# Performance work log

Measured on AMD Instinct MI355X. Metric: run time of the kernel, lower is better.

## Reference

```python
import jax, jax.numpy as jnp
import numpy as np

B, P, ENC, EMB, DEC, ATT, V = 64, 196, 512, 512, 512, 512, 10000
CLS_E, NCLS = 512, 200
MAX_LEN = 52
MAX_T = MAX_LEN - 1  # decode steps = max(caption_lengths) - 1


def setup_inputs() -> dict:
    key = jax.random.key(0)
    ks = jax.random.split(key, 24)
    s = 0.02
    u = lambda k, shp: jax.random.uniform(k, shp, jnp.float32, -0.1, 0.1)
    n = lambda k, shp: jax.random.normal(k, shp, jnp.float32) * s
    cap_len = jax.random.randint(ks[2], (B, 1), 2, MAX_LEN + 1)
    cap_len = cap_len.at[0, 0].set(MAX_LEN)  # ensure max decode length is static MAX_T
    return {
        "encoder_out": jax.random.normal(ks[0], (B, P, ENC), jnp.float32),
        "encoded_captions": jax.random.randint(ks[1], (B, MAX_LEN), 0, V),
        "caption_lengths": cap_len,
        "class_k": jax.random.randint(ks[3], (B, 1), 0, NCLS),
        "emb_W": u(ks[4], (V, EMB)),
        "cls_emb_W": u(ks[5], (NCLS, CLS_E)),
        "enc_att_W": n(ks[6], (ENC, ATT)), "enc_att_b": jnp.zeros((ATT,), jnp.float32),
        "dec_att_W": n(ks[7], (DEC, ATT)), "dec_att_b": jnp.zeros((ATT,), jnp.float32),
        "full_att_w": n(ks[8], (ATT,)), "full_att_b": jnp.zeros((), jnp.float32),
        "init_h_W": n(ks[9], (ENC + CLS_E, DEC)), "init_h_b": jnp.zeros((DEC,), jnp.float32),
        "init_c_W": n(ks[10], (ENC + CLS_E, DEC)), "init_c_b": jnp.zeros((DEC,), jnp.float32),
        "f_beta_W": n(ks[11], (DEC, ENC)), "f_beta_b": jnp.zeros((ENC,), jnp.float32),
        "lstm_Wih": n(ks[12], (4 * DEC, EMB + ENC + CLS_E)),
        "lstm_Whh": n(ks[13], (4 * DEC, DEC)),
        "lstm_bih": jnp.zeros((4 * DEC,), jnp.float32),
        "lstm_bhh": jnp.zeros((4 * DEC,), jnp.float32),
        "fc_W": u(ks[14], (DEC, V)), "fc_b": jnp.zeros((V,), jnp.float32),
    }


def reference(encoder_out, encoded_captions, caption_lengths, class_k,
              emb_W, cls_emb_W, enc_att_W, enc_att_b, dec_att_W, dec_att_b,
              full_att_w, full_att_b, init_h_W, init_h_b, init_c_W, init_c_b,
              f_beta_W, f_beta_b, lstm_Wih, lstm_Whh, lstm_bih, lstm_bhh,
              fc_W, fc_b):
    # Sort by descending caption length (torch: caption_lengths.sort(descending=True))
    lens = caption_lengths[:, 0]
    sort_ind = jnp.argsort(-lens)
    lens_s = lens[sort_ind]
    enc = encoder_out[sort_ind]              # [B,P,ENC]
    caps = encoded_captions[sort_ind]        # [B,L]
    embs = emb_W[caps]                       # [B,L,EMB]
    # NOTE: original code does NOT sort class_k -- faithful to that.
    cls_emb = cls_emb_W[class_k[:, 0]]       # [B,CLS_E] (class_embedding[:,0,:])
    dec_len = lens_s - 1                     # decode_lengths

    init_in = jnp.concatenate([enc.mean(axis=1), cls_emb], axis=1)
    h = init_in @ init_h_W + init_h_b        # [B,DEC]
    c = init_in @ init_c_W + init_c_b
    att1 = enc @ enc_att_W + enc_att_b       # [B,P,ATT] (same every step in torch)

    def step(carry, xs):
        h, c = carry
        emb_t, t = xs                        # emb_t: [B,EMB]
        active = (t < dec_len)[:, None]      # ragged batch_size_t truncation as mask
        # attention
        att2 = h @ dec_att_W + dec_att_b
        e = jnp.einsum('bpa,a->bp', jax.nn.relu(att1 + att2[:, None, :]), full_att_w) + full_att_b
        alpha = jax.nn.softmax(e, axis=1)
        awe = jnp.einsum('bpe,bp->be', enc, alpha)
        gate = jax.nn.sigmoid(h @ f_beta_W + f_beta_b)
        awe = gate * awe
        # LSTMCell (torch gate order: i, f, g, o)
        x = jnp.concatenate([emb_t, awe, cls_emb], axis=1)
        gates = x @ lstm_Wih.T + lstm_bih + h @ lstm_Whh.T + lstm_bhh
        i_, f_, g_, o_ = jnp.split(gates, 4, axis=1)
        c_new = jax.nn.sigmoid(f_) * c + jax.nn.sigmoid(i_) * jnp.tanh(g_)
        h_new = jax.nn.sigmoid(o_) * jnp.tanh(c_new)
        # dropout is inference-mode identity
        pred = jnp.where(active, h_new @ fc_W + fc_b, 0.0)
        h = jnp.where(active, h_new, h)
        c = jnp.where(active, c_new, c)
        return (h, c), pred

    xs = (embs[:, :MAX_T].transpose(1, 0, 2), jnp.arange(MAX_T))
    _, preds = jax.lax.scan(step, (h, c), xs)
    predictions = preds.transpose(1, 0, 2)   # [B,MAX_T,V]
    return predictions, caps, dec_len, sort_ind
```

## Files before the change

kernel.cpp:

```cpp
#include <hip/hip_runtime.h>
#include <cstddef>
#include <cstdint>
#include <math.h>

#define BB 64
#define PP 196
#define ENCD 512
#define DECD 512
#define ATTD 512
#define VOC 10000
#define CLSE 512
#define MAXLEN 52
#define MAXT 51
#define G4 2048
#define XDIM 1536

#define OFF_PRED 0
#define OFF_CAPS (BB * MAXT * VOC)
#define OFF_DECLEN (OFF_CAPS + BB * MAXLEN)
#define OFF_SORT (OFF_DECLEN + BB)

static constexpr size_t W_SORT   = 0;
static constexpr size_t W_DECLEN = 64;
static constexpr size_t W_CAPS   = 128;
static constexpr size_t W_CLS    = 3584;
static constexpr size_t W_H      = W_CLS + BB * CLSE;
static constexpr size_t W_C      = W_H + BB * DECD;
static constexpr size_t W_ININ   = W_C + BB * DECD;
static constexpr size_t W_Z      = W_ININ + BB * 1024;
static constexpr size_t W_AWE    = W_Z + BB * 3072;
static constexpr size_t W_CLSPRE = W_AWE + BB * ENCD;
static constexpr size_t W_W1P    = W_CLSPRE + BB * G4;
static constexpr size_t W_W2P    = W_W1P + (size_t)256 * 12 * 512;
static constexpr size_t W_HALL   = W_W2P + (size_t)256 * 8 * 1024;
static constexpr size_t W_ATT1   = W_HALL + (size_t)BB * MAXT * DECD;
static constexpr size_t W_CNT    = W_ATT1 + (size_t)BB * PP * ATTD;
static constexpr size_t W_PAWE   = W_CNT + 3264;

__device__ __forceinline__ float sigm(float x) { return 1.f / (1.f + expf(-x)); }

__device__ __forceinline__ double cohLd(const double* p) {
    return __hip_atomic_load(p, __ATOMIC_RELAXED, __HIP_MEMORY_SCOPE_AGENT);
}
__device__ __forceinline__ float cohLdF(const float* p) {
    return __hip_atomic_load(p, __ATOMIC_RELAXED, __HIP_MEMORY_SCOPE_AGENT);
}
__device__ __forceinline__ void cohSt(double* p, double v) {
    __hip_atomic_store(p, v, __ATOMIC_RELAXED, __HIP_MEMORY_SCOPE_AGENT);
}
__device__ __forceinline__ void cohStF(float* p, float v) {
    __hip_atomic_store(p, v, __ATOMIC_RELAXED, __HIP_MEMORY_SCOPE_AGENT);
}

__global__ void setup_kernel(const int* __restrict__ cap_len, float* __restrict__ out,
                             int* __restrict__ sortind, int* __restrict__ declen,
                             int* __restrict__ cnt) {
    __shared__ int sl[BB];
    int i = threadIdx.x;
    for (int k = i; k < 3264; k += 64) cnt[k] = 0;
    sl[i] = cap_len[i];
    __syncthreads();
    int li = sl[i];
    int rank = 0;
    for (int j = 0; j < BB; j++) {
        int lj = sl[j];
        rank += (lj > li) || (lj == li && j < i);
    }
    sortind[rank] = i;
    declen[rank] = li - 1;
    out[OFF_SORT + rank] = (float)i;
    out[OFF_DECLEN + rank] = (float)(li - 1);
}

__global__ void gather_kernel(const int* __restrict__ ecaps, const int* __restrict__ classk,
                              const float* __restrict__ clsW, const int* __restrict__ sortind,
                              int* __restrict__ caps_i, float* __restrict__ cls,
                              float* __restrict__ out) {
    int idx = blockIdx.x * 256 + threadIdx.x;
    if (idx < BB * MAXLEN) {
        int b = idx / MAXLEN, t2 = idx - b * MAXLEN;
        int sb = sortind[b];
        int v = ecaps[sb * MAXLEN + t2];
        caps_i[idx] = v;
        out[OFF_CAPS + idx] = (float)v;
    }
    int j = idx - BB * MAXLEN;
    if (j >= 0 && j < BB * CLSE) {
        int row = j >> 9, k = j & 511;
        int ck = classk[row];
        cls[j] = clsW[ck * CLSE + k];
    }
}

__global__ void mean_cls_kernel(const float* __restrict__ enc, const float* __restrict__ cls,
                                const int* __restrict__ sortind, float* __restrict__ initin) {
    int b = blockIdx.x;
    int sb = sortind[b];
    for (int k = threadIdx.x; k < ENCD; k += 256) {
        const float* ep = enc + (size_t)sb * PP * ENCD + k;
        float s = 0.f;
        for (int p = 0; p < PP; p++) s += ep[(size_t)p * ENCD];
        initin[b * 1024 + k] = s * (1.f / 196.f);
        initin[b * 1024 + 512 + k] = cls[b * CLSE + k];
    }
}

__global__ void init_hc_kernel(const float* __restrict__ initin,
                               const float* __restrict__ hW, const float* __restrict__ hb,
                               const float* __restrict__ cW, const float* __restrict__ cb,
                               float* __restrict__ h, float* __restrict__ c) {
    int gid = blockIdx.x * 256 + threadIdx.x;
    int j = gid & 511, b = (gid >> 9) & 63, which = gid >> 15;
    const float* W = which ? cW : hW;
    const float* bias = which ? cb : hb;
    const float* x = initin + b * 1024;
    float acc = bias[j];
    for (int k = 0; k < 1024; k++) acc += x[k] * W[(size_t)k * 512 + j];
    (which ? c : h)[b * 512 + j] = acc;
}

__global__ void pack_w1p_kernel(const float* __restrict__ dA, const float* __restrict__ fB,
                                const float* __restrict__ whh, float* __restrict__ W1p) {
    int gid = blockIdx.x * 256 + threadIdx.x;
    int k = gid & 511, cc = (gid >> 9) % 12, jb = gid / (512 * 12);
    int q = jb * 12 + cc;
    float v;
    if (q < 512) v = dA[k * 512 + q];
    else if (q < 1024) v = fB[k * 512 + (q - 512)];
    else v = whh[(size_t)(q - 1024) * 512 + k];
    W1p[gid] = v;
}

__global__ void pack_w2p_kernel(const float* __restrict__ wih, float* __restrict__ W2p) {
    int gid = blockIdx.x * 256 + threadIdx.x;
    int k = gid & 1023, cc = (gid >> 10) & 7, jb = gid >> 13;
    int gcol = 512 * (cc >> 1) + 2 * jb + (cc & 1);
    W2p[gid] = wih[(size_t)gcol * XDIM + k];
}

__global__ __launch_bounds__(256)
void att1_kernel(const float* __restrict__ enc, const float* __restrict__ Wa,
                 const float* __restrict__ ba, const int* __restrict__ sortind,
                 float* __restrict__ att1) {
    __shared__ float As[16][66];
    __shared__ float Bs[16][64];
    int tid = threadIdx.x;
    int n0 = blockIdx.x * 64, m0 = blockIdx.y * 64;
    int tx = tid & 15, ty = tid >> 4;
    int lm = tid >> 2, lk4 = (tid & 3) * 4;
    int bkk = tid >> 4, bnn4 = (tid & 15) * 4;
    int gm = m0 + lm;
    int b = gm / PP, p = gm - b * PP;
    int sb = sortind[b];
    const float* arow = enc + ((size_t)sb * PP + p) * ENCD;
    float acc[4][4] = {};
    for (int k0 = 0; k0 < ENCD; k0 += 16) {
        float4 av = *(const float4*)(arow + k0 + lk4);
        float4 bv = *(const float4*)(Wa + (size_t)(k0 + bkk) * 512 + n0 + bnn4);
        __syncthreads();
        As[lk4 + 0][lm] = av.x; As[lk4 + 1][lm] = av.y;
        As[lk4 + 2][lm] = av.z; As[lk4 + 3][lm] = av.w;
        *(float4*)&Bs[bkk][bnn4] = bv;
        __syncthreads();
#pragma unroll
        for (int kk = 0; kk < 16; kk++) {
            float a[4], bq[4];
#pragma unroll
            for (int i = 0; i < 4; i++) a[i] = As[kk][ty * 4 + i];
#pragma unroll
            for (int jj = 0; jj < 4; jj++) bq[jj] = Bs[kk][tx * 4 + jj];
#pragma unroll
            for (int i = 0; i < 4; i++)
#pragma unroll
                for (int jj = 0; jj < 4; jj++) acc[i][jj] += a[i] * bq[jj];
        }
    }
#pragma unroll
    for (int i = 0; i < 4; i++) {
        int m = m0 + ty * 4 + i;
        int n = n0 + tx * 4;
        float4 o;
        o.x = acc[i][0] + ba[n + 0];
        o.y = acc[i][1] + ba[n + 1];
        o.z = acc[i][2] + ba[n + 2];
        o.w = acc[i][3] + ba[n + 3];
        *(float4*)(att1 + (size_t)m * ATTD + n) = o;
    }
}

__global__ __launch_bounds__(256)
void clspre_kernel(const float* __restrict__ cls, const float* __restrict__ wih,
                   const float* __restrict__ bih, const float* __restrict__ bhh,
                   float* __restrict__ clspre) {
    __shared__ float As[16][66];
    __shared__ float Bs[16][68];
    int tid = threadIdx.x;
    int n0 = blockIdx.x * 64;
    int tx = tid & 15, ty = tid >> 4;
    int lm = tid >> 2, lk4 = (tid & 3) * 4;
    int bnn = tid & 63, bkk4 = (tid >> 6) * 4;
    float acc[4][4] = {};
    for (int k0 = 0; k0 < 512; k0 += 16) {
        float4 av = *(const float4*)(cls + lm * CLSE + k0 + lk4);
        float4 bv = *(const float4*)(wih + (size_t)(n0 + bnn) * XDIM + 1024 + k0 + bkk4);
        __syncthreads();
        As[lk4 + 0][lm] = av.x; As[lk4 + 1][lm] = av.y;
        As[lk4 + 2][lm] = av.z; As[lk4 + 3][lm] = av.w;
        Bs[bkk4 + 0][bnn] = bv.x; Bs[bkk4 + 1][bnn] = bv.y;
        Bs[bkk4 + 2][bnn] = bv.z; Bs[bkk4 + 3][bnn] = bv.w;
        __syncthreads();
#pragma unroll
        for (int kk = 0; kk < 16; kk++) {
            float a[4], bq[4];
#pragma unroll
            for (int i = 0; i < 4; i++) a[i] = As[kk][ty * 4 + i];
#pragma unroll
            for (int jj = 0; jj < 4; jj++) bq[jj] = Bs[kk][tx * 4 + jj];
#pragma unroll
            for (int i = 0; i < 4; i++)
#pragma unroll
                for (int jj = 0; jj < 4; jj++) acc[i][jj] += a[i] * bq[jj];
        }
    }
#pragma unroll
    for (int i = 0; i < 4; i++) {
        int m = ty * 4 + i;
#pragma unroll
        for (int jj = 0; jj < 4; jj++) {
            int n = n0 + tx * 4 + jj;
            clspre[m * G4 + n] = acc[i][jj] + bih[n] + bhh[n];
        }
    }
}

__global__ __launch_bounds__(256)
void zstep_kernel(const float* __restrict__ hG, const float* __restrict__ W1p,
                  const float* __restrict__ dab, const float* __restrict__ fbb,
                  float* __restrict__ Zg) {
    const int j = blockIdx.x, tid = threadIdx.x;
    const int lane = tid & 63, wvid = tid >> 6;
    __shared__ float stage[64 * 132];
    __shared__ float W1res[12 * 516];

    for (int idx = tid; idx < 1536; idx += 256) {
        int cc = idx >> 7, pos = (idx & 127) << 2;
        *(float4*)&W1res[cc * 516 + pos] = *(const float4*)&W1p[(size_t)j * 6144 + cc * 512 + pos];
    }
    const int gc0 = j * 12 + wvid, gc1 = gc0 + 4, gc2 = gc0 + 8;
    const float bias0 = (gc0 < 512) ? dab[gc0] : ((gc0 < 1024) ? fbb[gc0 - 512] : 0.f);
    const float bias1 = (gc1 < 512) ? dab[gc1] : ((gc1 < 1024) ? fbb[gc1 - 512] : 0.f);
    const float bias2 = (gc2 < 512) ? dab[gc2] : ((gc2 < 1024) ? fbb[gc2 - 512] : 0.f);

    float a0 = 0.f, a1 = 0.f, a2 = 0.f;
    for (int ch = 0; ch < 4; ch++) {
        __syncthreads();
        {
            const float4* hp = (const float4*)(hG + ((size_t)lane << 9) + (ch << 7) + (wvid << 5));
            float4 tmp[8];
#pragma unroll
            for (int i = 0; i < 8; i++) tmp[i] = hp[i];
#pragma unroll
            for (int i = 0; i < 8; i++)
                *(float4*)&stage[lane * 132 + (wvid << 5) + (i << 2)] = tmp[i];
        }
        __syncthreads();
        const float* sp  = &stage[lane * 132];
        const float* w0p = &W1res[wvid * 516 + (ch << 7)];
        const float* w1p = &W1res[(wvid + 4) * 516 + (ch << 7)];
        const float* w2p = &W1res[(wvid + 8) * 516 + (ch << 7)];
#pragma unroll 8
        for (int kk = 0; kk < 128; kk += 4) {
            float4 av = *(const float4*)(sp + kk);
            float4 u0 = *(const float4*)(w0p + kk);
            float4 u1 = *(const float4*)(w1p + kk);
            float4 u2 = *(const float4*)(w2p + kk);
            a0 = fmaf(av.x, u0.x, fmaf(av.y, u0.y, fmaf(av.z, u0.z, fmaf(av.w, u0.w, a0))));
            a1 = fmaf(av.x, u1.x, fmaf(av.y, u1.y, fmaf(av.z, u1.z, fmaf(av.w, u1.w, a1))));
            a2 = fmaf(av.x, u2.x, fmaf(av.y, u2.y, fmaf(av.z, u2.z, fmaf(av.w, u2.w, a2))));
        }
    }
    Zg[lane * 3072 + gc0] = a0 + bias0;
    Zg[lane * 3072 + gc1] = a1 + bias1;
    Zg[lane * 3072 + gc2] = a2 + bias2;
}

__global__ __launch_bounds__(256)
void attq_kernel(const float* __restrict__ att1g, const float* __restrict__ encg,
                 const float* __restrict__ Zg, const float* __restrict__ fullw,
                 const float* __restrict__ fullb, const int* __restrict__ sortind,
                 const int* __restrict__ declen, float* __restrict__ paweG,
                 int* __restrict__ cntG, float* __restrict__ aweG, int t) {
    const int blk = blockIdx.x;
    const int b = blk >> 2, q = blk & 3;
    if (t >= declen[b]) return;
    const int tid = threadIdx.x;
    const int lane = tid & 63, wvid = tid >> 6;

    __shared__ float att2s[512];
    __shared__ float esS[52];
    __shared__ float redA[1], redB[1];
    __shared__ float pawe[4 * 520];
    __shared__ int finS;

    {
        float2 v = *(const float2*)&Zg[b * 3072 + 2 * tid];
        *(float2*)&att2s[2 * tid] = v;
    }
    __syncthreads();

    const float fbv = fullb[0];
    {
        float4 t0 = *(const float4*)&att2s[lane * 8];
        float4 t1 = *(const float4*)&att2s[lane * 8 + 4];
        float4 w0 = *(const float4*)&fullw[lane * 8];
        float4 w1 = *(const float4*)&fullw[lane * 8 + 4];
        const float* a1b = att1g + (size_t)b * PP * 512;
        for (int lp = wvid; lp < 49; lp += 4) {
            int p = 49 * q + lp;
            const float4* ar = (const float4*)(a1b + (size_t)p * 512) + lane * 2;
            float4 u0 = ar[0], u1 = ar[1];
            float s = fmaxf(u0.x + t0.x, 0.f) * w0.x + fmaxf(u0.y + t0.y, 0.f) * w0.y
                    + fmaxf(u0.z + t0.z, 0.f) * w0.z + fmaxf(u0.w + t0.w, 0.f) * w0.w
                    + fmaxf(u1.x + t1.x, 0.f) * w1.x + fmaxf(u1.y + t1.y, 0.f) * w1.y
                    + fmaxf(u1.z + t1.z, 0.f) * w1.z + fmaxf(u1.w + t1.w, 0.f) * w1.w;
#pragma unroll
            for (int off = 32; off; off >>= 1) s += __shfl_down(s, off, 64);
            if (lane == 0) esS[lp] = s + fbv;
        }
    }
    __syncthreads();
    if (tid < 64) {
        float v = (tid < 49) ? esS[tid] : -1e30f;
#pragma unroll
        for (int off = 32; off; off >>= 1) v = fmaxf(v, __shfl_down(v, off, 64));
        if (tid == 0) redA[0] = v;
    }
    __syncthreads();
    const float mq = redA[0];
    if (tid < 64) {
        float ev = (tid < 49) ? expf(esS[tid] - mq) : 0.f;
        float sv = ev;
#pragma unroll
        for (int off = 32; off; off >>= 1) sv += __shfl_down(sv, off, 64);
        if (tid == 0) redB[0] = sv;
        if (tid < 49) esS[tid] = ev;
    }
    __syncthreads();
    const float Sq = redB[0];

    const int sb = sortind[b];
    {
        float aw[8] = {};
        const float* encb = encg + (size_t)sb * PP * 512 + lane;
        for (int lp = wvid; lp < 49; lp += 4) {
            int p = 49 * q + lp;
            float al = esS[lp];
            const float* ep = encb + (size_t)p * 512;
#pragma unroll
            for (int i = 0; i < 8; i++) aw[i] = fmaf(al, ep[i << 6], aw[i]);
        }
#pragma unroll
        for (int i = 0; i < 8; i++) pawe[wvid * 520 + (i << 6) + lane] = aw[i];
    }
    __syncthreads();
    {
        const int k2 = 2 * tid;
        const int base = ((b << 2) + q) * 520;
        float s0 = pawe[k2] + pawe[520 + k2] + pawe[2 * 520 + k2] + pawe[3 * 520 + k2];
        float s1 = pawe[k2 + 1] + pawe[520 + k2 + 1] + pawe[2 * 520 + k2 + 1] + pawe[3 * 520 + k2 + 1];
        double d;
        *(float2*)&d = make_float2(s0, s1);
        cohSt((double*)&paweG[base + k2], d);
        if (tid == 0) {
            cohStF(&paweG[base + 512], Sq);
            cohStF(&paweG[base + 513], mq);
        }
    }
    __syncthreads();

    if (tid == 0) {
        int prev = __hip_atomic_fetch_add(&cntG[t * 64 + b], 1,
                                          __ATOMIC_RELAXED, __HIP_MEMORY_SCOPE_AGENT);
        finS = (prev == 3);
    }
    __syncthreads();
    if (finS) {
        float mv[4], sv[4];
#pragma unroll
        for (int qq = 0; qq < 4; qq++) {
            mv[qq] = cohLdF(&paweG[((b << 2) + qq) * 520 + 513]);
            sv[qq] = cohLdF(&paweG[((b << 2) + qq) * 520 + 512]);
        }
        float M = fmaxf(fmaxf(mv[0], mv[1]), fmaxf(mv[2], mv[3]));
        float f0 = expf(mv[0] - M), f1 = expf(mv[1] - M);
        float f2 = expf(mv[2] - M), f3 = expf(mv[3] - M);
        float inv = 1.f / (sv[0] * f0 + sv[1] * f1 + sv[2] * f2 + sv[3] * f3);
        const int k2 = 2 * tid;
        const double* pd = (const double*)paweG;
        float a0 = 0.f, a1 = 0.f;
        {
            double d0 = cohLd(pd + ((b << 2) + 0) * 260 + tid);
            double d1 = cohLd(pd + ((b << 2) + 1) * 260 + tid);
            double d2 = cohLd(pd + ((b << 2) + 2) * 260 + tid);
            double d3 = cohLd(pd + ((b << 2) + 3) * 260 + tid);
            float2 g0 = *(float2*)&d0, g1 = *(float2*)&d1;
            float2 g2 = *(float2*)&d2, g3 = *(float2*)&d3;
            a0 = g0.x * f0 + g1.x * f1 + g2.x * f2 + g3.x * f3;
            a1 = g0.y * f0 + g1.y * f1 + g2.y * f2 + g3.y * f3;
        }
        float2 gv = *(const float2*)&Zg[b * 3072 + 512 + k2];
        float2 o = make_float2(a0 * inv * sigm(gv.x), a1 * inv * sigm(gv.y));
        *(float2*)&aweG[b * 512 + k2] = o;
    }
}

__global__ __launch_bounds__(256)
void gatestep_kernel(const float* __restrict__ embW, const float* __restrict__ W2p,
                     const float* __restrict__ clspreg, const float* __restrict__ Zg,
                     const float* __restrict__ aweG, const int* __restrict__ caps_i,
                     const int* __restrict__ declen, float* __restrict__ hG,
                     float* __restrict__ cG, float* __restrict__ hall, int t) {
    const int j = blockIdx.x, tid = threadIdx.x;
    const int lane = tid & 63, wvid = tid >> 6;
    const int d0 = j * 2;
    __shared__ float stage[64 * 132];
    __shared__ float W2res[8 * 1028];
    __shared__ float Gs[8 * 66];
    __shared__ float hhS[64 * 8];
    __shared__ float CsS[64 * 8];
    __shared__ int capS[64];
    __shared__ int declen_s[64];

    for (int idx = tid; idx < 2048; idx += 256) {
        int cc = idx >> 8, pos = (idx & 255) << 2;
        *(float4*)&W2res[cc * 1028 + pos] = *(const float4*)&W2p[(size_t)j * 8192 + cc * 1024 + pos];
    }
    for (int idx = tid; idx < 512; idx += 256) {
        int r = idx >> 3, cc = idx & 7;
        CsS[idx] = clspreg[(r << 11) + ((cc >> 1) << 9) + d0 + (cc & 1)];
    }
    if (tid < 64) { capS[tid] = caps_i[tid * MAXLEN + t]; declen_s[tid] = declen[tid]; }
    {
        int r = tid >> 2, g = tid & 3;
        float2 v = *(const float2*)&Zg[r * 3072 + 1024 + (g << 9) + d0];
        hhS[(r << 3) + (g << 1)] = v.x;
        hhS[(r << 3) + (g << 1) + 1] = v.y;
    }

    float ac0 = 0.f, ac1 = 0.f;
    for (int ch = 0; ch < 8; ch++) {
        __syncthreads();
        {
            const float4* src = (ch < 4)
                ? (const float4*)(embW + ((size_t)capS[lane] << 9) + (ch << 7) + (wvid << 5))
                : (const float4*)(aweG + ((size_t)lane << 9) + ((ch - 4) << 7) + (wvid << 5));
            float4 tmp[8];
#pragma unroll
            for (int i = 0; i < 8; i++) tmp[i] = src[i];
#pragma unroll
            for (int i = 0; i < 8; i++)
                *(float4*)&stage[lane * 132 + (wvid << 5) + (i << 2)] = tmp[i];
        }
        __syncthreads();
        const float* sp  = &stage[lane * 132];
        const float* v0p = &W2res[wvid * 1028 + (ch << 7)];
        const float* v1p = &W2res[(wvid + 4) * 1028 + (ch << 7)];
#pragma unroll 8
        for (int kk = 0; kk < 128; kk += 4) {
            float4 av = *(const float4*)(sp + kk);
            float4 u0 = *(const float4*)(v0p + kk);
            float4 u1 = *(const float4*)(v1p + kk);
            ac0 = fmaf(av.x, u0.x, fmaf(av.y, u0.y, fmaf(av.z, u0.z, fmaf(av.w, u0.w, ac0))));
            ac1 = fmaf(av.x, u1.x, fmaf(av.y, u1.y, fmaf(av.z, u1.z, fmaf(av.w, u1.w, ac1))));
        }
    }
    Gs[wvid * 66 + lane]       = ac0 + CsS[(lane << 3) + wvid]     + hhS[(lane << 3) + wvid];
    Gs[(wvid + 4) * 66 + lane] = ac1 + CsS[(lane << 3) + wvid + 4] + hhS[(lane << 3) + wvid + 4];
    __syncthreads();
    if (tid < 128) {
        int r2 = tid & 63, dd = tid >> 6;
        if (t < declen_s[r2]) {
            float iv = Gs[(0 + dd) * 66 + r2];
            float fv = Gs[(2 + dd) * 66 + r2];
            float gv = Gs[(4 + dd) * 66 + r2];
            float ov = Gs[(6 + dd) * 66 + r2];
            float cold = cG[r2 * 512 + d0 + dd];
            float cn = sigm(fv) * cold + sigm(iv) * tanhf(gv);
            float hn = sigm(ov) * tanhf(cn);
            cG[r2 * 512 + d0 + dd] = cn;
            hG[r2 * 512 + d0 + dd] = hn;
            hall[((size_t)r2 * MAXT + t) * 512 + d0 + dd] = hn;
        }
    }
}

__global__ __launch_bounds__(256)
void fc_kernel(const float* __restrict__ hall, const float* __restrict__ fcW,
               const float* __restrict__ fcb, const int* __restrict__ declen,
               float* __restrict__ out) {
    __shared__ float As[16][66];
    __shared__ float Bs[16][68];
    int tid = threadIdx.x;
    int n0 = blockIdx.x * 64, m0 = blockIdx.y * 64;
    int tx = tid & 15, ty = tid >> 4;
    int lm = tid >> 2, lk4 = (tid & 3) * 4;
    int bkk = tid >> 4, bnn4 = (tid & 15) * 4;
    const float* arow = hall + (size_t)(m0 + lm) * DECD;
    bool nfull = (n0 + 64 <= VOC);
    float acc[4][4] = {};
    for (int k0 = 0; k0 < 512; k0 += 16) {
        float4 av = *(const float4*)(arow + k0 + lk4);
        float4 bv;
        if (nfull) {
            bv = *(const float4*)(fcW + (size_t)(k0 + bkk) * VOC + n0 + bnn4);
        } else {
            const float* bp = fcW + (size_t)(k0 + bkk) * VOC;
            int nb = n0 + bnn4;
            bv.x = (nb + 0 < VOC) ? bp[nb + 0] : 0.f;
            bv.y = (nb + 1 < VOC) ? bp[nb + 1] : 0.f;
            bv.z = (nb + 2 < VOC) ? bp[nb + 2] : 0.f;
            bv.w = (nb + 3 < VOC) ? bp[nb + 3] : 0.f;
        }
        __syncthreads();
        As[lk4 + 0][lm] = av.x; As[lk4 + 1][lm] = av.y;
        As[lk4 + 2][lm] = av.z; As[lk4 + 3][lm] = av.w;
        *(float4*)&Bs[bkk][bnn4] = bv;
        __syncthreads();
#pragma unroll
        for (int kk = 0; kk < 16; kk++) {
            float a[4], bq[4];
#pragma unroll
            for (int i = 0; i < 4; i++) a[i] = As[kk][ty * 4 + i];
#pragma unroll
            for (int jj = 0; jj < 4; jj++) bq[jj] = Bs[kk][tx * 4 + jj];
#pragma unroll
            for (int i = 0; i < 4; i++)
#pragma unroll
                for (int jj = 0; jj < 4; jj++) acc[i][jj] += a[i] * bq[jj];
        }
    }
#pragma unroll
    for (int i = 0; i < 4; i++) {
        int m = m0 + ty * 4 + i;
        int b = m / MAXT, t = m - b * MAXT;
        bool act = t < declen[b];
        int n = n0 + tx * 4;
        if (nfull) {
            float4 o;
            o.x = act ? acc[i][0] + fcb[n + 0] : 0.f;
            o.y = act ? acc[i][1] + fcb[n + 1] : 0.f;
            o.z = act ? acc[i][2] + fcb[n + 2] : 0.f;
            o.w = act ? acc[i][3] + fcb[n + 3] : 0.f;
            *(float4*)(out + (size_t)m * VOC + n) = o;
        } else {
#pragma unroll
            for (int jj = 0; jj < 4; jj++) {
                int nn = n + jj;
                if (nn < VOC) out[(size_t)m * VOC + nn] = act ? acc[i][jj] + fcb[nn] : 0.f;
            }
        }
    }
}

extern "C" void kernel_launch(void* const* d_in, const int* in_sizes, int n_in,
                              void* d_out, int out_size, void* d_ws, size_t ws_size,
                              hipStream_t stream) {
    const float* enc     = (const float*)d_in[0];
    const int*   ecaps   = (const int*)d_in[1];
    const int*   lens    = (const int*)d_in[2];
    const int*   classk  = (const int*)d_in[3];
    const float* embW    = (const float*)d_in[4];
    const float* clsW    = (const float*)d_in[5];
    const float* encattW = (const float*)d_in[6];
    const float* encattb = (const float*)d_in[7];
    const float* decattW = (const float*)d_in[8];
    const float* decattb = (const float*)d_in[9];
    const float* fullw   = (const float*)d_in[10];
    const float* fullb   = (const float*)d_in[11];
    const float* ihW     = (const float*)d_in[12];
    const float* ihb     = (const float*)d_in[13];
    const float* icW     = (const float*)d_in[14];
    const float* icb     = (const float*)d_in[15];
    const float* fbW     = (const float*)d_in[16];
    const float* fbb     = (const float*)d_in[17];
    const float* Wih     = (const float*)d_in[18];
    const float* Whh     = (const float*)d_in[19];
    const float* bih     = (const float*)d_in[20];
    const float* bhh     = (const float*)d_in[21];
    const float* fcW     = (const float*)d_in[22];
    const float* fcb     = (const float*)d_in[23];

    float* out = (float*)d_out;
    float* ws  = (float*)d_ws;
    int*   wsi = (int*)d_ws;

    int*   sortind = wsi + W_SORT;
    int*   declen  = wsi + W_DECLEN;
    int*   caps_i  = wsi + W_CAPS;
    float* cls     = ws + W_CLS;
    float* h       = ws + W_H;
    float* c       = ws + W_C;
    float* initin  = ws + W_ININ;
    float* Z       = ws + W_Z;
    float* awe     = ws + W_AWE;
    float* clspre  = ws + W_CLSPRE;
    float* W1p     = ws + W_W1P;
    float* W2p     = ws + W_W2P;
    float* hall    = ws + W_HALL;
    float* att1    = ws + W_ATT1;
    int*   cnt     = wsi + W_CNT;
    float* pawe    = ws + W_PAWE;

    setup_kernel<<<1, 64, 0, stream>>>(lens, out, sortind, declen, cnt);
    gather_kernel<<<141, 256, 0, stream>>>(ecaps, classk, clsW, sortind, caps_i, cls, out);
    mean_cls_kernel<<<BB, 256, 0, stream>>>(enc, cls, sortind, initin);
    init_hc_kernel<<<256, 256, 0, stream>>>(initin, ihW, ihb, icW, icb, h, c);
    pack_w1p_kernel<<<6144, 256, 0, stream>>>(decattW, fbW, Whh, W1p);
    pack_w2p_kernel<<<8192, 256, 0, stream>>>(Wih, W2p);
    att1_kernel<<<dim3(8, 196), 256, 0, stream>>>(enc, encattW, encattb, sortind, att1);
    clspre_kernel<<<32, 256, 0, stream>>>(cls, Wih, bih, bhh, clspre);

    for (int t = 0; t < MAXT; t++) {
        zstep_kernel<<<256, 256, 0, stream>>>(h, W1p, decattb, fbb, Z);
        attq_kernel<<<256, 256, 0, stream>>>(att1, enc, Z, fullw, fullb,
                                             sortind, declen, pawe, cnt, awe, t);
        gatestep_kernel<<<256, 256, 0, stream>>>(embW, W2p, clspre, Z, awe,
                                                 caps_i, declen, h, c, hall, t);
    }

    fc_kernel<<<dim3(157, 51), 256, 0, stream>>>(hall, fcW, fcb, declen, out);
}
```

Before: 3.914 ms.

## Precompute embedding gate contributions for all steps; prefetch staged chunks in step kernels

Adds an embpre kernel that computes the embedding part of the LSTM input projection for all decode steps up front as one batched GEMM, folding in the class and bias term. The per-step gate kernel then only handles the attention-weighted-encoding half, halving its weight staging and chunk loop. It also prefetches the next global chunk into registers while the current chunk is staged in zstep and gatestep, and switches the small GEMM kernels to float4 LDS reads with padded rows. The new path depends on the workspace being large enough, about 26 MB extra, and falls back to the old path otherwise.

```diff
diff --git a/kernel.cpp b/kernel.cpp
--- a/kernel.cpp
+++ b/kernel.cpp
@@ -36,6 +36,8 @@
 static constexpr size_t W_ATT1   = W_HALL + (size_t)BB * MAXT * DECD;
 static constexpr size_t W_CNT    = W_ATT1 + (size_t)BB * PP * ATTD;
 static constexpr size_t W_PAWE   = W_CNT + 3264;
+static constexpr size_t W_CPRE2  = W_PAWE + (size_t)BB * 4 * 520;
+static constexpr size_t W_END    = W_CPRE2 + (size_t)MAXT * BB * G4;
 
 __device__ __forceinline__ float sigm(float x) { return 1.f / (1.f + expf(-x)); }
 
@@ -142,7 +144,7 @@
 void att1_kernel(const float* __restrict__ enc, const float* __restrict__ Wa,
                  const float* __restrict__ ba, const int* __restrict__ sortind,
                  float* __restrict__ att1) {
-    __shared__ float As[16][66];
+    __shared__ float As[16][68];
     __shared__ float Bs[16][64];
     int tid = threadIdx.x;
     int n0 = blockIdx.x * 64, m0 = blockIdx.y * 64;
@@ -164,15 +166,16 @@
         __syncthreads();
 #pragma unroll
         for (int kk = 0; kk < 16; kk++) {
-            float a[4], bq[4];
-#pragma unroll
-            for (int i = 0; i < 4; i++) a[i] = As[kk][ty * 4 + i];
-#pragma unroll
-            for (int jj = 0; jj < 4; jj++) bq[jj] = Bs[kk][tx * 4 + jj];
-#pragma unroll
-            for (int i = 0; i < 4; i++)
-#pragma unroll
-                for (int jj = 0; jj < 4; jj++) acc[i][jj] += a[i] * bq[jj];
+            float4 a4 = *(const float4*)&As[kk][ty * 4];
+            float4 b4 = *(const float4*)&Bs[kk][tx * 4];
+            acc[0][0] = fmaf(a4.x, b4.x, acc[0][0]); acc[0][1] = fmaf(a4.x, b4.y, acc[0][1]);
+            acc[0][2] = fmaf(a4.x, b4.z, acc[0][2]); acc[0][3] = fmaf(a4.x, b4.w, acc[0][3]);
+            acc[1][0] = fmaf(a4.y, b4.x, acc[1][0]); acc[1][1] = fmaf(a4.y, b4.y, acc[1][1]);
+            acc[1][2] = fmaf(a4.y, b4.z, acc[1][2]); acc[1][3] = fmaf(a4.y, b4.w, acc[1][3]);
+            acc[2][0] = fmaf(a4.z, b4.x, acc[2][0]); acc[2][1] = fmaf(a4.z, b4.y, acc[2][1]);
+            acc[2][2] = fmaf(a4.z, b4.z, acc[2][2]); acc[2][3] = fmaf(a4.z, b4.w, acc[2][3]);
+            acc[3][0] = fmaf(a4.w, b4.x, acc[3][0]); acc[3][1] = fmaf(a4.w, b4.y, acc[3][1]);
+            acc[3][2] = fmaf(a4.w, b4.z, acc[3][2]); acc[3][3] = fmaf(a4.w, b4.w, acc[3][3]);
         }
     }
 #pragma unroll
@@ -192,7 +195,7 @@
 void clspre_kernel(const float* __restrict__ cls, const float* __restrict__ wih,
                    const float* __restrict__ bih, const float* __restrict__ bhh,
                    float* __restrict__ clspre) {
-    __shared__ float As[16][66];
+    __shared__ float As[16][68];
     __shared__ float Bs[16][68];
     int tid = threadIdx.x;
     int n0 = blockIdx.x * 64;
@@ -211,15 +214,16 @@
         __syncthreads();
 #pragma unroll
         for (int kk = 0; kk < 16; kk++) {
-            float a[4], bq[4];
-#pragma unroll
-            for (int i = 0; i < 4; i++) a[i] = As[kk][ty * 4 + i];
-#pragma unroll
-            for (int jj = 0; jj < 4; jj++) bq[jj] = Bs[kk][tx * 4 + jj];
-#pragma unroll
-            for (int i = 0; i < 4; i++)
-#pragma unroll
-                for (int jj = 0; jj < 4; jj++) acc[i][jj] += a[i] * bq[jj];
+            float4 a4 = *(const float4*)&As[kk][ty * 4];
+            float4 b4 = *(const float4*)&Bs[kk][tx * 4];
+            acc[0][0] = fmaf(a4.x, b4.x, acc[0][0]); acc[0][1] = fmaf(a4.x, b4.y, acc[0][1]);
+            acc[0][2] = fmaf(a4.x, b4.z, acc[0][2]); acc[0][3] = fmaf(a4.x, b4.w, acc[0][3]);
+            acc[1][0] = fmaf(a4.y, b4.x, acc[1][0]); acc[1][1] = fmaf(a4.y, b4.y, acc[1][1]);
+            acc[1][2] = fmaf(a4.y, b4.z, acc[1][2]); acc[1][3] = fmaf(a4.y, b4.w, acc[1][3]);
+            acc[2][0] = fmaf(a4.z, b4.x, acc[2][0]); acc[2][1] = fmaf(a4.z, b4.y, acc[2][1]);
+            acc[2][2] = fmaf(a4.z, b4.z, acc[2][2]); acc[2][3] = fmaf(a4.z, b4.w, acc[2][3]);
+            acc[3][0] = fmaf(a4.w, b4.x, acc[3][0]); acc[3][1] = fmaf(a4.w, b4.y, acc[3][1]);
+            acc[3][2] = fmaf(a4.w, b4.z, acc[3][2]); acc[3][3] = fmaf(a4.w, b4.w, acc[3][3]);
         }
     }
 #pragma unroll
@@ -230,6 +234,55 @@
             int n = n0 + tx * 4 + jj;
             clspre[m * G4 + n] = acc[i][jj] + bih[n] + bhh[n];
         }
+    }
+}
+
+__global__ __launch_bounds__(256)
+void embpre_kernel(const float* __restrict__ embW, const float* __restrict__ wih,
+                   const float* __restrict__ clspreg, const int* __restrict__ caps_i,
+                   float* __restrict__ cpre2) {
+    __shared__ float As[16][68];
+    __shared__ float Bs[16][68];
+    int tid = threadIdx.x;
+    int n0 = blockIdx.x * 64, t = blockIdx.y;
+    int tx = tid & 15, ty = tid >> 4;
+    int lm = tid >> 2, lk4 = (tid & 3) * 4;
+    int bnn = tid & 63, bkk4 = (tid >> 6) * 4;
+    const int cap = caps_i[lm * MAXLEN + t];
+    const float* arow = embW + ((size_t)cap << 9);
+    float acc[4][4] = {};
+    for (int k0 = 0; k0 < 512; k0 += 16) {
+        float4 av = *(const float4*)(arow + k0 + lk4);
+        float4 bv = *(const float4*)(wih + (size_t)(n0 + bnn) * XDIM + k0 + bkk4);
+        __syncthreads();
+        As[lk4 + 0][lm] = av.x; As[lk4 + 1][lm] = av.y;
+        As[lk4 + 2][lm] = av.z; As[lk4 + 3][lm] = av.w;
+        Bs[bkk4 + 0][bnn] = bv.x; Bs[bkk4 + 1][bnn] = bv.y;
+        Bs[bkk4 + 2][bnn] = bv.z; Bs[bkk4 + 3][bnn] = bv.w;
+        __syncthreads();
+#pragma unroll
+        for (int kk = 0; kk < 16; kk++) {
+            float4 a4 = *(const float4*)&As[kk][ty * 4];
+            float4 b4 = *(const float4*)&Bs[kk][tx * 4];
+            acc[0][0] = fmaf(a4.x, b4.x, acc[0][0]); acc[0][1] = fmaf(a4.x, b4.y, acc[0][1]);
+            acc[0][2] = fmaf(a4.x, b4.z, acc[0][2]); acc[0][3] = fmaf(a4.x, b4.w, acc[0][3]);
+            acc[1][0] = fmaf(a4.y, b4.x, acc[1][0]); acc[1][1] = fmaf(a4.y, b4.y, acc[1][1]);
+            acc[1][2] = fmaf(a4.y, b4.z, acc[1][2]); acc[1][3] = fmaf(a4.y, b4.w, acc[1][3]);
+            acc[2][0] = fmaf(a4.z, b4.x, acc[2][0]); acc[2][1] = fmaf(a4.z, b4.y, acc[2][1]);
+            acc[2][2] = fmaf(a4.z, b4.z, acc[2][2]); acc[2][3] = fmaf(a4.z, b4.w, acc[2][3]);
+            acc[3][0] = fmaf(a4.w, b4.x, acc[3][0]); acc[3][1] = fmaf(a4.w, b4.y, acc[3][1]);
+            acc[3][2] = fmaf(a4.w, b4.z, acc[3][2]); acc[3][3] = fmaf(a4.w, b4.w, acc[3][3]);
+        }
+    }
+#pragma unroll
+    for (int i = 0; i < 4; i++) {
+        int bl = ty * 4 + i;
+        int n = n0 + tx * 4;
+        float4 cp = *(const float4*)&clspreg[bl * G4 + n];
+        float4 o;
+        o.x = acc[i][0] + cp.x; o.y = acc[i][1] + cp.y;
+        o.z = acc[i][2] + cp.z; o.w = acc[i][3] + cp.w;
+        *(float4*)&cpre2[((size_t)t * 64 + bl) * G4 + n] = o;
     }
 }
 
@@ -251,19 +304,25 @@
     const float bias1 = (gc1 < 512) ? dab[gc1] : ((gc1 < 1024) ? fbb[gc1 - 512] : 0.f);
     const float bias2 = (gc2 < 512) ? dab[gc2] : ((gc2 < 1024) ? fbb[gc2 - 512] : 0.f);
 
+    float4 cur[8];
+    {
+        const float4* hp = (const float4*)(hG + ((size_t)lane << 9) + (wvid << 5));
+#pragma unroll
+        for (int i = 0; i < 8; i++) cur[i] = hp[i];
+    }
     float a0 = 0.f, a1 = 0.f, a2 = 0.f;
+#pragma unroll
     for (int ch = 0; ch < 4; ch++) {
         __syncthreads();
-        {
-            const float4* hp = (const float4*)(hG + ((size_t)lane << 9) + (ch << 7) + (wvid << 5));
-            float4 tmp[8];
-#pragma unroll
-            for (int i = 0; i < 8; i++) tmp[i] = hp[i];
-#pragma unroll
-            for (int i = 0; i < 8; i++)
-                *(float4*)&stage[lane * 132 + (wvid << 5) + (i << 2)] = tmp[i];
-        }
-        __syncthreads();
+#pragma unroll
+        for (int i = 0; i < 8; i++)
+            *(float4*)&stage[lane * 132 + (wvid << 5) + (i << 2)] = cur[i];
+        __syncthreads();
+        if (ch < 3) {
+            const float4* hp = (const float4*)(hG + ((size_t)lane << 9) + ((ch + 1) << 7) + (wvid << 5));
+#pragma unroll
+            for (int i = 0; i < 8; i++) cur[i] = hp[i];
+        }
         const float* sp  = &stage[lane * 132];
         const float* w0p = &W1res[wvid * 516 + (ch << 7)];
         const float* w1p = &W1res[(wvid + 4) * 516 + (ch << 7)];
@@ -414,15 +473,18 @@
     }
 }
 
+template<int PRE>
 __global__ __launch_bounds__(256)
 void gatestep_kernel(const float* __restrict__ embW, const float* __restrict__ W2p,
-                     const float* __restrict__ clspreg, const float* __restrict__ Zg,
+                     const float* __restrict__ cpre, const float* __restrict__ Zg,
                      const float* __restrict__ aweG, const int* __restrict__ caps_i,
                      const int* __restrict__ declen, float* __restrict__ hG,
                      float* __restrict__ cG, float* __restrict__ hall, int t) {
     const int j = blockIdx.x, tid = threadIdx.x;
     const int lane = tid & 63, wvid = tid >> 6;
     const int d0 = j * 2;
+    const int NCH = PRE ? 4 : 8;
+    const int WST = PRE ? 516 : 1028;
     __shared__ float stage[64 * 132];
     __shared__ float W2res[8 * 1028];
     __shared__ float Gs[8 * 66];
@@ -431,40 +493,64 @@
     __shared__ int capS[64];
     __shared__ int declen_s[64];
 
-    for (int idx = tid; idx < 2048; idx += 256) {
-        int cc = idx >> 8, pos = (idx & 255) << 2;
-        *(float4*)&W2res[cc * 1028 + pos] = *(const float4*)&W2p[(size_t)j * 8192 + cc * 1024 + pos];
+    if (PRE) {
+        for (int idx = tid; idx < 1024; idx += 256) {
+            int cc = idx >> 7, pos = (idx & 127) << 2;
+            *(float4*)&W2res[cc * 516 + pos] =
+                *(const float4*)&W2p[(size_t)j * 8192 + cc * 1024 + 512 + pos];
+        }
+    } else {
+        for (int idx = tid; idx < 2048; idx += 256) {
+            int cc = idx >> 8, pos = (idx & 255) << 2;
+            *(float4*)&W2res[cc * 1028 + pos] =
+                *(const float4*)&W2p[(size_t)j * 8192 + cc * 1024 + pos];
+        }
     }
     for (int idx = tid; idx < 512; idx += 256) {
         int r = idx >> 3, cc = idx & 7;
-        CsS[idx] = clspreg[(r << 11) + ((cc >> 1) << 9) + d0 + (cc & 1)];
-    }
-    if (tid < 64) { capS[tid] = caps_i[tid * MAXLEN + t]; declen_s[tid] = declen[tid]; }
+        CsS[idx] = cpre[(r << 11) + ((cc >> 1) << 9) + d0 + (cc & 1)];
+    }
+    if (tid < 64) {
+        if (!PRE) capS[tid] = caps_i[tid * MAXLEN + t];
+        declen_s[tid] = declen[tid];
+    }
     {
         int r = tid >> 2, g = tid & 3;
         float2 v = *(const float2*)&Zg[r * 3072 + 1024 + (g << 9) + d0];
         hhS[(r << 3) + (g << 1)] = v.x;
         hhS[(r << 3) + (g << 1) + 1] = v.y;
     }
-
+    if (!PRE) __syncthreads();
+
+    float4 cur[8];
+    {
+        const float4* src = PRE
+            ? (const float4*)(aweG + ((size_t)lane << 9) + (wvid << 5))
+            : (const float4*)(embW + ((size_t)capS[lane] << 9) + (wvid << 5));
+#pragma unroll
+        for (int i = 0; i < 8; i++) cur[i] = src[i];
+    }
     float ac0 = 0.f, ac1 = 0.f;
-    for (int ch = 0; ch < 8; ch++) {
-        __syncthreads();
-        {
-            const float4* src = (ch < 4)
-                ? (const float4*)(embW + ((size_t)capS[lane] << 9) + (ch << 7) + (wvid << 5))
-                : (const float4*)(aweG + ((size_t)lane << 9) + ((ch - 4) << 7) + (wvid << 5));
-            float4 tmp[8];
-#pragma unroll
-            for (int i = 0; i < 8; i++) tmp[i] = src[i];
-#pragma unroll
-            for (int i = 0; i < 8; i++)
-                *(float4*)&stage[lane * 132 + (wvid << 5) + (i << 2)] = tmp[i];
-        }
-        __syncthreads();
+#pragma unroll
+    for (int ch = 0; ch < NCH; ch++) {
+        __syncthreads();
+#pragma unroll
+        for (int i = 0; i < 8; i++)
+            *(float4*)&stage[lane * 132 + (wvid << 5) + (i << 2)] = cur[i];
+        __syncthreads();
+        if (ch + 1 < NCH) {
+            int cn = ch + 1;
+            const float4* src;
+            if (PRE) src = (const float4*)(aweG + ((size_t)lane << 9) + (cn << 7) + (wvid << 5));
+            else src = (cn < 4)
+                ? (const float4*)(embW + ((size_t)capS[lane] << 9) + (cn << 7) + (wvid << 5))
+                : (const float4*)(aweG + ((size_t)lane << 9) + ((cn - 4) << 7) + (wvid << 5));
+#pragma unroll
+            for (int i = 0; i < 8; i++) cur[i] = src[i];
+        }
         const float* sp  = &stage[lane * 132];
-        const float* v0p = &W2res[wvid * 1028 + (ch << 7)];
-        const float* v1p = &W2res[(wvid + 4) * 1028 + (ch << 7)];
+        const float* v0p = &W2res[wvid * WST + (ch << 7)];
+        const float* v1p = &W2res[(wvid + 4) * WST + (ch << 7)];
 #pragma unroll 8
         for (int kk = 0; kk < 128; kk += 4) {
             float4 av = *(const float4*)(sp + kk);
@@ -498,7 +584,7 @@
 void fc_kernel(const float* __restrict__ hall, const float* __restrict__ fcW,
                const float* __restrict__ fcb, const int* __restrict__ declen,
                float* __restrict__ out) {
-    __shared__ float As[16][66];
+    __shared__ float As[16][68];
     __shared__ float Bs[16][68];
     int tid = threadIdx.x;
     int n0 = blockIdx.x * 64, m0 = blockIdx.y * 64;
@@ -528,15 +614,16 @@
         __syncthreads();
 #pragma unroll
         for (int kk = 0; kk < 16; kk++) {
-            float a[4], bq[4];
-#pragma unroll
-            for (int i = 0; i < 4; i++) a[i] = As[kk][ty * 4 + i];
-#pragma unroll
-            for (int jj = 0; jj < 4; jj++) bq[jj] = Bs[kk][tx * 4 + jj];
-#pragma unroll
-            for (int i = 0; i < 4; i++)
-#pragma unroll
-                for (int jj = 0; jj < 4; jj++) acc[i][jj] += a[i] * bq[jj];
+            float4 a4 = *(const float4*)&As[kk][ty * 4];
+            float4 b4 = *(const float4*)&Bs[kk][tx * 4];
+            acc[0][0] = fmaf(a4.x, b4.x, acc[0][0]); acc[0][1] = fmaf(a4.x, b4.y, acc[0][1]);
+            acc[0][2] = fmaf(a4.x, b4.z, acc[0][2]); acc[0][3] = fmaf(a4.x, b4.w, acc[0][3]);
+            acc[1][0] = fmaf(a4.y, b4.x, acc[1][0]); acc[1][1] = fmaf(a4.y, b4.y, acc[1][1]);
+            acc[1][2] = fmaf(a4.y, b4.z, acc[1][2]); acc[1][3] = fmaf(a4.y, b4.w, acc[1][3]);
+            acc[2][0] = fmaf(a4.z, b4.x, acc[2][0]); acc[2][1] = fmaf(a4.z, b4.y, acc[2][1]);
+            acc[2][2] = fmaf(a4.z, b4.z, acc[2][2]); acc[2][3] = fmaf(a4.z, b4.w, acc[2][3]);
+            acc[3][0] = fmaf(a4.w, b4.x, acc[3][0]); acc[3][1] = fmaf(a4.w, b4.y, acc[3][1]);
+            acc[3][2] = fmaf(a4.w, b4.z, acc[3][2]); acc[3][3] = fmaf(a4.w, b4.w, acc[3][3]);
         }
     }
 #pragma unroll
@@ -610,6 +697,9 @@
     float* att1    = ws + W_ATT1;
     int*   cnt     = wsi + W_CNT;
     float* pawe    = ws + W_PAWE;
+    float* cpre2   = ws + W_CPRE2;
+
+    const bool pre = ws_size >= W_END * 4;
 
     setup_kernel<<<1, 64, 0, stream>>>(lens, out, sortind, declen, cnt);
     gather_kernel<<<141, 256, 0, stream>>>(ecaps, classk, clsW, sortind, caps_i, cls, out);
@@ -619,13 +709,19 @@
     pack_w2p_kernel<<<8192, 256, 0, stream>>>(Wih, W2p);
     att1_kernel<<<dim3(8, 196), 256, 0, stream>>>(enc, encattW, encattb, sortind, att1);
     clspre_kernel<<<32, 256, 0, stream>>>(cls, Wih, bih, bhh, clspre);
+    if (pre)
+        embpre_kernel<<<dim3(32, 51), 256, 0, stream>>>(embW, Wih, clspre, caps_i, cpre2);
 
     for (int t = 0; t < MAXT; t++) {
         zstep_kernel<<<256, 256, 0, stream>>>(h, W1p, decattb, fbb, Z);
         attq_kernel<<<256, 256, 0, stream>>>(att1, enc, Z, fullw, fullb,
                                              sortind, declen, pawe, cnt, awe, t);
-        gatestep_kernel<<<256, 256, 0, stream>>>(embW, W2p, clspre, Z, awe,
-                                                 caps_i, declen, h, c, hall, t);
+        if (pre)
+            gatestep_kernel<1><<<256, 256, 0, stream>>>(embW, W2p,
+                cpre2 + (size_t)t * 64 * G4, Z, awe, caps_i, declen, h, c, hall, t);
+        else
+            gatestep_kernel<0><<<256, 256, 0, stream>>>(embW, W2p,
+                clspre, Z, awe, caps_i, declen, h, c, hall, t);
     }
 
     fc_kernel<<<dim3(157, 51), 256, 0, stream>>>(hall, fcW, fcb, declen, out);
```

Measured after the change: 3.998 ms. +2.1%, slower.
